# Performance work log

Hardware: AMD Instinct MI355X
Metric: run time of the kernel (lower is better)

The kernel has to match this reference:

```python
import jax, jax.numpy as jnp
import numpy as np

N, T0, T1, C = 65536, 128, 64, 16
MIN_NEAR = 0.05


def _searchsorted(a, v):
    # batched right-side searchsorted over last dim
    return jax.vmap(lambda aa, vv: jnp.searchsorted(aa, vv, side='right'))(a, v)


def contract(x):
    # MERF-style contraction, x: [..., 3]
    ax = jnp.abs(x)
    mag = jnp.max(ax, axis=-1, keepdims=True)              # [..., 1]
    idx = jnp.argmax(ax, axis=-1)                          # [...]
    oh = jnp.arange(x.shape[-1]) == idx[..., None]         # one-hot of max axis
    inv = 1.0 / mag
    scale = jnp.where(oh, (2.0 - inv) * inv, inv)
    return jnp.where(mag < 1.0, x, x * scale)


def sample_pdf(bins, weights, T):
    # bins: [N, T0+1], weights: [N, T0] -> new bins [N, T]
    n, t0 = weights.shape
    w = weights + 0.01
    pdf = w / jnp.sum(w, -1, keepdims=True)
    cdf = jnp.minimum(jnp.cumsum(pdf, -1), 1.0)
    cdf = jnp.concatenate([jnp.zeros_like(cdf[..., :1]), cdf], -1)  # [N, T0+1]
    u = jnp.linspace(0.5 / T, 1.0 - 0.5 / T, T, dtype=bins.dtype)
    u = jnp.broadcast_to(u, (n, T))
    inds = _searchsorted(cdf, u)
    below = jnp.clip(inds - 1, 0, t0)
    above = jnp.clip(inds, 0, t0)
    g = lambda a, i: jnp.take_along_axis(a, i, axis=-1)
    cdf0, cdf1 = g(cdf, below), g(cdf, above)
    b0, b1 = g(bins, below), g(bins, above)
    t = jnp.clip(jnp.nan_to_num((u - cdf0) / (cdf1 - cdf0)), 0.0, 1.0)
    return b0 + t * (b1 - b0)


def compute_weights(real_bins, sigmas):
    deltas = real_bins[..., 1:] - real_bins[..., :-1]
    ds = deltas * sigmas
    alphas = 1.0 - jnp.exp(-ds)
    trans = jnp.exp(-jnp.concatenate(
        [jnp.zeros_like(ds[..., :1]), jnp.cumsum(ds[..., :-1], -1)], -1))
    return jnp.nan_to_num(alphas * trans)


def loss_interlevel(t0, w0, t1, w1):
    cw1 = jnp.concatenate([jnp.zeros_like(w1[..., :1]), jnp.cumsum(w1, -1)], -1)
    hi_clip = w1.shape[-1] - 1
    inds_lo = jnp.clip(_searchsorted(t1[..., :-1], t0[..., :-1]) - 1, 0, hi_clip)
    inds_hi = jnp.clip(_searchsorted(t1[..., 1:], t0[..., 1:]), 0, hi_clip)
    cw1_lo = jnp.take_along_axis(cw1[..., :-1], inds_lo, axis=-1)
    cw1_hi = jnp.take_along_axis(cw1[..., 1:], inds_hi, axis=-1)
    w = cw1_hi - cw1_lo
    return jnp.maximum(w0 - w, 0.0) ** 2 / (w0 + 1e-8)


def eff_distloss(w, m, interval):
    # efficient O(T) distortion loss (torch_efficient_distloss)
    loss_uni = (1.0 / 3.0) * jnp.mean(jnp.sum(interval * w ** 2, -1))
    wm = w * m
    w_cs = jnp.cumsum(w, -1)
    wm_cs = jnp.cumsum(wm, -1)
    loss_bi = 2.0 * jnp.mean(jnp.sum(
        wm[..., 1:] * w_cs[..., :-1] - w[..., 1:] * wm_cs[..., :-1], -1))
    return loss_uni + loss_bi


def setup_inputs():
    key = jax.random.key(0)
    ks = jax.random.split(key, 8)
    rays_o = 0.1 * jax.random.normal(ks[0], (N, 3), jnp.float32)
    rd = jax.random.normal(ks[1], (N, 3), jnp.float32)
    rays_d = rd / jnp.linalg.norm(rd, axis=-1, keepdims=True)
    aabb = jnp.array([-2.0, -2.0, -2.0, 2.0, 2.0, 2.0], jnp.float32)
    sigmas_coarse = 5.0 * jax.random.uniform(ks[2], (N, T0), jnp.float32)
    sigmas_fine = 5.0 * jax.random.uniform(ks[3], (N, T1), jnp.float32)
    colors = jax.random.uniform(ks[4], (N, T1, C), jnp.float32)
    w_view = 0.1 * jax.random.normal(ks[5], (C, 3), jnp.float32)
    b_view = jnp.zeros((3,), jnp.float32)
    return dict(rays_o=rays_o, rays_d=rays_d, aabb=aabb,
                sigmas_coarse=sigmas_coarse, sigmas_fine=sigmas_fine,
                colors=colors, w_view=w_view, b_view=b_view)


def reference(rays_o, rays_d, aabb, sigmas_coarse, sigmas_fine, colors, w_view, b_view):
    # near/far from aabb
    tmin = (aabb[:3] - rays_o) / (rays_d + 1e-15)
    tmax = (aabb[3:] - rays_o) / (rays_d + 1e-15)
    near = jnp.max(jnp.minimum(tmin, tmax), -1, keepdims=True)
    far = jnp.min(jnp.maximum(tmin, tmax), -1, keepdims=True)
    bad = far < near
    near = jnp.maximum(jnp.where(bad, 1e9, near), MIN_NEAR)
    far = jnp.where(bad, 1e9, far)

    spacing = lambda x: jnp.where(x < 1.0, x / 2.0, 1.0 - 1.0 / (2.0 * x))
    spacing_inv = lambda x: jnp.where(x < 0.5, 2.0 * x, 1.0 / (2.0 - 2.0 * x))
    s_near, s_far = spacing(near), spacing(far)

    # coarse (proposal) level: uniform bins in warped space
    bins0 = jnp.broadcast_to(jnp.linspace(0.0, 1.0, T0 + 1, dtype=rays_o.dtype), (N, T0 + 1))
    real_bins0 = spacing_inv(s_near * (1.0 - bins0) + s_far * bins0)
    weights0 = compute_weights(real_bins0, sigmas_coarse)

    # fine level: inverse-CDF sampling (detached in original)
    bins1 = sample_pdf(jax.lax.stop_gradient(bins0),
                       jax.lax.stop_gradient(weights0), T1 + 1)
    real_bins1 = spacing_inv(s_near * (1.0 - bins1) + s_far * bins1)
    rays_t = 0.5 * (real_bins1[..., 1:] + real_bins1[..., :-1])      # [N, T1]
    xyzs = rays_o[:, None, :] + rays_d[:, None, :] * rays_t[..., None]
    xyzs = contract(xyzs)                                            # [N, T1, 3]
    weights1 = compute_weights(real_bins1, sigmas_fine)

    weights_sum = jnp.sum(weights1, -1)                              # [N]
    depth = jnp.sum(weights1 * rays_t, -1)                           # [N]
    f_image = jnp.sum(weights1[..., None] * colors, -2)              # [N, C]
    image = jax.nn.sigmoid(f_image @ w_view + b_view)                # [N, 3]
    image = image + (1.0 - weights_sum)[:, None] * 1.0               # bg_color = 1
    f_xyz = jnp.sum(weights1[..., None] * xyzs, -2)                  # [N, 3]

    prop_loss = jnp.mean(loss_interlevel(
        jax.lax.stop_gradient(bins1), jax.lax.stop_gradient(weights1),
        bins0, weights0))
    intervals = bins1[..., 1:] - bins1[..., :-1]
    mids = bins1[..., :-1] + intervals / 2.0
    dist_loss = eff_distloss(weights1, mids, intervals)

    return image, depth, f_xyz, prop_loss, dist_loss
```

## Files before the change

kernel.cpp:

```cpp
#include <hip/hip_runtime.h>
#include <math.h>

#define NRAYS 65536
#define T0N 128
#define T1N 64
#define CN 16
#define RPB 4
#define NBLK (NRAYS / RPB)

#define IMG_OFF   0
#define DEPTH_OFF (NRAYS * 3)
#define FXYZ_OFF  (NRAYS * 4)
#define PROP_OFF  (NRAYS * 7)
#define DIST_OFF  (NRAYS * 7 + 1)

__device__ __forceinline__ float wave_sum(float x) {
#pragma unroll
  for (int off = 1; off < 64; off <<= 1) x += __shfl_xor(x, off, 64);
  return x;
}

__device__ __forceinline__ float scan_incl(float x, int lane) {
#pragma unroll
  for (int off = 1; off < 64; off <<= 1) {
    float y = __shfl_up(x, off, 64);
    if (lane >= off) x += y;
  }
  return x;
}

__device__ __forceinline__ float spacing_fn(float x) {
  return (x < 1.0f) ? (x * 0.5f) : (1.0f - 1.0f / (2.0f * x));
}
__device__ __forceinline__ float spacing_inv_fn(float x) {
  return (x < 0.5f) ? (2.0f * x) : (1.0f / (2.0f - 2.0f * x));
}

__device__ __forceinline__ int ss_right(const float* a, int n, float v) {
  int lo = 0, hi = n;
  while (lo < hi) {
    int m = (lo + hi) >> 1;
    if (a[m] <= v) lo = m + 1; else hi = m;
  }
  return lo;
}

__global__ void __launch_bounds__(256) nerf_main(
    const float* __restrict__ rays_o, const float* __restrict__ rays_d,
    const float* __restrict__ aabb, const float* __restrict__ sig_c,
    const float* __restrict__ sig_f, const float* __restrict__ colors,
    const float* __restrict__ w_view, const float* __restrict__ b_view,
    float* __restrict__ out, float* __restrict__ ws_partials, int use_atomic) {
  __shared__ float s_cdf[RPB][129 + 1];
  __shared__ float s_bins1[RPB][66];
  __shared__ float s_rb1[RPB][66];
  __shared__ float s_w1[RPB][64];
  __shared__ float s_cw1[RPB][66];
  __shared__ float s_fimg[RPB][16];
  __shared__ float s_scal[RPB][2];

  const int wv = threadIdx.x >> 6;
  const int lane = threadIdx.x & 63;
  const int ray = blockIdx.x * RPB + wv;

  float ro[3], rd[3];
#pragma unroll
  for (int c = 0; c < 3; ++c) { ro[c] = rays_o[ray * 3 + c]; rd[c] = rays_d[ray * 3 + c]; }
  float near = -3.0e38f, far = 3.0e38f;
#pragma unroll
  for (int c = 0; c < 3; ++c) {
    float dd = rd[c] + 1e-15f;
    float ta = (aabb[c] - ro[c]) / dd;
    float tb = (aabb[c + 3] - ro[c]) / dd;
    near = fmaxf(near, fminf(ta, tb));
    far = fminf(far, fmaxf(ta, tb));
  }
  if (far < near) { near = 1e9f; far = 1e9f; }
  near = fmaxf(near, 0.05f);
  const float s_near = spacing_fn(near), s_far = spacing_fn(far);

  const int i0 = 2 * lane, i1 = 2 * lane + 1;
  const float b_a = (float)i0 * (1.0f / 128.0f);
  const float b_b = (float)i1 * (1.0f / 128.0f);
  const float b_c = (float)(i1 + 1) * (1.0f / 128.0f);
  const float rb_a = spacing_inv_fn(s_near * (1.0f - b_a) + s_far * b_a);
  const float rb_b = spacing_inv_fn(s_near * (1.0f - b_b) + s_far * b_b);
  const float rb_c = spacing_inv_fn(s_near * (1.0f - b_c) + s_far * b_c);
  const float2 sg = ((const float2*)sig_c)[ray * 64 + lane];
  const float ds0 = (rb_b - rb_a) * sg.x;
  const float ds1 = (rb_c - rb_b) * sg.y;
  {
  }
  float pr = ds0 + ds1;
  float Spr = scan_incl(pr, lane);
  float E0 = Spr - pr;
  float w00 = (1.0f - expf(-ds0)) * expf(-E0);
  float w01 = (1.0f - expf(-ds1)) * expf(-(E0 + ds0));
  if (w00 != w00) w00 = 0.0f;
  if (w01 != w01) w01 = 0.0f;

  const float wp0 = w00 + 0.01f, wp1 = w01 + 0.01f;
  const float tot = wave_sum(wp0 + wp1);
  const float pdf0 = wp0 / tot, pdf1 = wp1 / tot;
  float prp = pdf0 + pdf1;
  float Sp = scan_incl(prp, lane);
  float Ep = Sp - prp;
  s_cdf[wv][i0 + 1] = fminf(Ep + pdf0, 1.0f);
  s_cdf[wv][i1 + 1] = fminf(Sp, 1.0f);
  if (lane == 0) s_cdf[wv][0] = 0.0f;
  __syncthreads();

  auto sample_one = [&](int j) {
    const float u = ((float)j + 0.5f) * (1.0f / 65.0f);
    int inds = ss_right(&s_cdf[wv][0], 129, u);
    int below = max(min(inds - 1, 128), 0);
    int above = min(inds, 128);
    float c0 = s_cdf[wv][below], c1 = s_cdf[wv][above];
    float b0 = (float)below * (1.0f / 128.0f);
    float b1 = (float)above * (1.0f / 128.0f);
    float t = (u - c0) / (c1 - c0);
    t = fminf(fmaxf(t, 0.0f), 1.0f);
    float bvv = b0 + t * (b1 - b0);
    s_bins1[wv][j] = bvv;
    s_rb1[wv][j] = spacing_inv_fn(s_near * (1.0f - bvv) + s_far * bvv);
  };
  sample_one(lane);
  if (lane == 63) sample_one(64);
  __syncthreads();

  const float rbl = s_rb1[wv][lane];
  const float rbl1 = s_rb1[wv][lane + 1];
  const float delta = rbl1 - rbl;
  const float sgf = sig_f[ray * 64 + lane];
  const float dsf = delta * sgf;
  const float Sf = scan_incl(dsf, lane);
  float w1 = (1.0f - expf(-dsf)) * expf(-(Sf - dsf));
  if (w1 != w1) w1 = 0.0f;
  const float tmid = 0.5f * (rbl + rbl1);

  float px = ro[0] + rd[0] * tmid;
  float py = ro[1] + rd[1] * tmid;
  float pz = ro[2] + rd[2] * tmid;
  float cx = px, cy = py, cz = pz;
  {
    float ax = fabsf(px), ay = fabsf(py), az = fabsf(pz);
    float mag = fmaxf(ax, fmaxf(ay, az));
    if (mag >= 1.0f) {
      float inv = 1.0f / mag;
      float so = (2.0f - inv) * inv;
      int idx = (ax >= ay && ax >= az) ? 0 : ((ay >= az) ? 1 : 2);
      cx = px * (idx == 0 ? so : inv);
      cy = py * (idx == 1 ? so : inv);
      cz = pz * (idx == 2 ? so : inv);
    }
  }

  const float wsum = wave_sum(w1);
  const float depth = wave_sum(w1 * tmid);
  const float fx = wave_sum(w1 * cx);
  const float fy = wave_sum(w1 * cy);
  const float fz = wave_sum(w1 * cz);

  s_w1[wv][lane] = w1;
  const float Scw = scan_incl(w1, lane);
  s_cw1[wv][lane + 1] = Scw;
  if (lane == 0) s_cw1[wv][0] = 0.0f;

  const float bl = s_bins1[wv][lane];
  const float bl1 = s_bins1[wv][lane + 1];
  const float interval = bl1 - bl;
  const float mid = bl + interval * 0.5f;
  const float wm = w1 * mid;
  const float Swm = scan_incl(wm, lane);
  const float w_excl = Scw - w1;
  const float wm_excl = Swm - wm;
  const float dl = (1.0f / 3.0f) * (interval * w1 * w1) + 2.0f * (wm * w_excl - w1 * wm_excl);
  const float dist_part = wave_sum(dl);
  __syncthreads();

  float prop_lane = 0.0f;
  {
    const float* b1p = &s_bins1[wv][0];
    const float* cwp = &s_cw1[wv][0];
#pragma unroll
    for (int k = 0; k < 2; ++k) {
      int i = 2 * lane + k;
      float w0v = (k == 0) ? w00 : w01;
      float vlo = (float)i * (1.0f / 128.0f);
      float vhi = (float)(i + 1) * (1.0f / 128.0f);
      int ilo = max(min(ss_right(b1p, 64, vlo) - 1, 63), 0);
      int ihi = min(ss_right(b1p + 1, 64, vhi), 63);
      float wint = cwp[ihi + 1] - cwp[ilo];
      float diff = fmaxf(w0v - wint, 0.0f);
      prop_lane += diff * diff / (w0v + 1e-8f);
    }
  }
  const float prop_part = wave_sum(prop_lane);

  {
    const int tg = lane >> 2, cg = lane & 3;
    const float4* col4 = (const float4*)(colors + (size_t)ray * (T1N * CN));
    float a0 = 0.f, a1 = 0.f, a2 = 0.f, a3 = 0.f;
#pragma unroll
    for (int it = 0; it < 4; ++it) {
      int t = tg + 16 * it;
      float wvv = s_w1[wv][t];
      float4 cvv = col4[t * 4 + cg];
      a0 = fmaf(wvv, cvv.x, a0);
      a1 = fmaf(wvv, cvv.y, a1);
      a2 = fmaf(wvv, cvv.z, a2);
      a3 = fmaf(wvv, cvv.w, a3);
    }
#pragma unroll
    for (int m = 4; m < 64; m <<= 1) {
      a0 += __shfl_xor(a0, m, 64);
      a1 += __shfl_xor(a1, m, 64);
      a2 += __shfl_xor(a2, m, 64);
      a3 += __shfl_xor(a3, m, 64);
    }
    if (lane < 4) {
      s_fimg[wv][lane * 4 + 0] = a0;
      s_fimg[wv][lane * 4 + 1] = a1;
      s_fimg[wv][lane * 4 + 2] = a2;
      s_fimg[wv][lane * 4 + 3] = a3;
    }
  }
  __syncthreads();

  if (lane < 3) {
    float acc = b_view[lane];
#pragma unroll
    for (int c = 0; c < 16; ++c) acc = fmaf(s_fimg[wv][c], w_view[c * 3 + lane], acc);
    out[IMG_OFF + ray * 3 + lane] = 1.0f / (1.0f + expf(-acc)) + (1.0f - wsum);
    out[FXYZ_OFF + ray * 3 + lane] = (lane == 0) ? fx : ((lane == 1) ? fy : fz);
  }
  if (lane == 0) {
    out[DEPTH_OFF + ray] = depth;
    s_scal[wv][0] = prop_part;
    s_scal[wv][1] = dist_part;
  }
  __syncthreads();
  if (threadIdx.x == 0) {
    float P = s_scal[0][0] + s_scal[1][0] + s_scal[2][0] + s_scal[3][0];
    float D = s_scal[0][1] + s_scal[1][1] + s_scal[2][1] + s_scal[3][1];
    if (use_atomic) {
      atomicAdd(out + PROP_OFF, P * (1.0f / ((float)NRAYS * 128.0f)));
      atomicAdd(out + DIST_OFF, D * (1.0f / (float)NRAYS));
    } else {
      ws_partials[blockIdx.x] = P;
      ws_partials[NBLK + blockIdx.x] = D;
    }
  }
}

__global__ void __launch_bounds__(256) reduce_partials(const float* __restrict__ ws,
                                                       float* __restrict__ out) {
  float p = 0.0f, d = 0.0f;
  for (int i = threadIdx.x; i < NBLK; i += 256) {
    p += ws[i];
    d += ws[NBLK + i];
  }
  p = wave_sum(p);
  d = wave_sum(d);
  __shared__ float sp[4], sd[4];
  const int wv = threadIdx.x >> 6, lane = threadIdx.x & 63;
  if (lane == 0) { sp[wv] = p; sd[wv] = d; }
  __syncthreads();
  if (threadIdx.x == 0) {
    float P = sp[0] + sp[1] + sp[2] + sp[3];
    float D = sd[0] + sd[1] + sd[2] + sd[3];
    out[PROP_OFF] = P * (1.0f / ((float)NRAYS * 128.0f));
    out[DIST_OFF] = D * (1.0f / (float)NRAYS);
  }
}

extern "C" void kernel_launch(void* const* d_in, const int* in_sizes, int n_in,
                              void* d_out, int out_size, void* d_ws, size_t ws_size,
                              hipStream_t stream) {
  const float* rays_o = (const float*)d_in[0];
  const float* rays_d = (const float*)d_in[1];
  const float* aabb = (const float*)d_in[2];
  const float* sig_c = (const float*)d_in[3];
  const float* sig_f = (const float*)d_in[4];
  const float* colors = (const float*)d_in[5];
  const float* w_view = (const float*)d_in[6];
  const float* b_view = (const float*)d_in[7];
  float* out = (float*)d_out;
  float* wsf = (float*)d_ws;

  const bool use_ws = (ws_size >= (size_t)(2 * NBLK) * sizeof(float)) && (wsf != nullptr);
  if (!use_ws) {
    hipMemsetAsync(out + PROP_OFF, 0, 2 * sizeof(float), stream);
  }
  nerf_main<<<NBLK, 256, 0, stream>>>(rays_o, rays_d, aabb, sig_c, sig_f, colors,
                                      w_view, b_view, out, wsf, use_ws ? 0 : 1);
  if (use_ws) reduce_partials<<<1, 256, 0, stream>>>(wsf, out);
}
```

Baseline: 439.5 us.

## Replace block barriers with wave-level syncs, shuffles, and early global loads

Each wavefront handles one ray, so the block-wide __syncthreads become wave barriers with an LDS fence. Several shared arrays are replaced by register shuffles: bins, real bins, w1 for the color sum, and f_image for the view projection. The colors and sigma loads are hoisted to the kernel start so their latency overlaps the coarse-pass math, and the normalization now reuses a single scan plus a reciprocal. Fast __expf replaces expf, which changes rounding slightly, and the partials reduction is vectorized.

```diff
diff --git a/kernel.cpp b/kernel.cpp
--- a/kernel.cpp
+++ b/kernel.cpp
@@ -29,6 +29,12 @@
   return x;
 }
 
+__device__ __forceinline__ void wave_lds_sync() {
+  __builtin_amdgcn_wave_barrier();
+  __builtin_amdgcn_fence(__ATOMIC_ACQ_REL, "workgroup");
+  __builtin_amdgcn_wave_barrier();
+}
+
 __device__ __forceinline__ float spacing_fn(float x) {
   return (x < 1.0f) ? (x * 0.5f) : (1.0f - 1.0f / (2.0f * x));
 }
@@ -51,17 +57,23 @@
     const float* __restrict__ sig_f, const float* __restrict__ colors,
     const float* __restrict__ w_view, const float* __restrict__ b_view,
     float* __restrict__ out, float* __restrict__ ws_partials, int use_atomic) {
-  __shared__ float s_cdf[RPB][129 + 1];
-  __shared__ float s_bins1[RPB][66];
-  __shared__ float s_rb1[RPB][66];
-  __shared__ float s_w1[RPB][64];
-  __shared__ float s_cw1[RPB][66];
-  __shared__ float s_fimg[RPB][16];
+  __shared__ float s_cdf[RPB][130];
+  __shared__ float s_bins1[RPB][65];
+  __shared__ float s_cw1[RPB][65];
   __shared__ float s_scal[RPB][2];
 
   const int wv = threadIdx.x >> 6;
   const int lane = threadIdx.x & 63;
   const int ray = blockIdx.x * RPB + wv;
+
+  const int tg = lane >> 2, cg = lane & 3;
+  const float4* col4 = (const float4*)(colors + (size_t)ray * (T1N * CN));
+  const float4 cva = col4[(tg + 0) * 4 + cg];
+  const float4 cvb = col4[(tg + 16) * 4 + cg];
+  const float4 cvc = col4[(tg + 32) * 4 + cg];
+  const float4 cvd = col4[(tg + 48) * 4 + cg];
+  const float2 sg = ((const float2*)sig_c)[ray * 64 + lane];
+  const float sgf = sig_f[ray * 64 + lane];
 
   float ro[3], rd[3];
 #pragma unroll
@@ -86,31 +98,28 @@
   const float rb_a = spacing_inv_fn(s_near * (1.0f - b_a) + s_far * b_a);
   const float rb_b = spacing_inv_fn(s_near * (1.0f - b_b) + s_far * b_b);
   const float rb_c = spacing_inv_fn(s_near * (1.0f - b_c) + s_far * b_c);
-  const float2 sg = ((const float2*)sig_c)[ray * 64 + lane];
   const float ds0 = (rb_b - rb_a) * sg.x;
   const float ds1 = (rb_c - rb_b) * sg.y;
-  {
-  }
-  float pr = ds0 + ds1;
-  float Spr = scan_incl(pr, lane);
-  float E0 = Spr - pr;
-  float w00 = (1.0f - expf(-ds0)) * expf(-E0);
-  float w01 = (1.0f - expf(-ds1)) * expf(-(E0 + ds0));
+  const float pr = ds0 + ds1;
+  const float Spr = scan_incl(pr, lane);
+  const float E0 = Spr - pr;
+  const float e0 = __expf(-E0);
+  const float ed0 = __expf(-ds0);
+  float w00 = (1.0f - ed0) * e0;
+  float w01 = (1.0f - __expf(-ds1)) * (e0 * ed0);
   if (w00 != w00) w00 = 0.0f;
   if (w01 != w01) w01 = 0.0f;
 
   const float wp0 = w00 + 0.01f, wp1 = w01 + 0.01f;
-  const float tot = wave_sum(wp0 + wp1);
-  const float pdf0 = wp0 / tot, pdf1 = wp1 / tot;
-  float prp = pdf0 + pdf1;
-  float Sp = scan_incl(prp, lane);
-  float Ep = Sp - prp;
-  s_cdf[wv][i0 + 1] = fminf(Ep + pdf0, 1.0f);
-  s_cdf[wv][i1 + 1] = fminf(Sp, 1.0f);
+  const float S2 = scan_incl(wp0 + wp1, lane);
+  const float tot = __shfl(S2, 63, 64);
+  const float rt = 1.0f / tot;
+  s_cdf[wv][i0 + 1] = fminf((S2 - wp1) * rt, 1.0f);
+  s_cdf[wv][i1 + 1] = fminf(S2 * rt, 1.0f);
   if (lane == 0) s_cdf[wv][0] = 0.0f;
-  __syncthreads();
-
-  auto sample_one = [&](int j) {
+  wave_lds_sync();
+
+  auto sample_one = [&](int j) -> float {
     const float u = ((float)j + 0.5f) * (1.0f / 65.0f);
     int inds = ss_right(&s_cdf[wv][0], 129, u);
     int below = max(min(inds - 1, 128), 0);
@@ -122,19 +131,19 @@
     t = fminf(fmaxf(t, 0.0f), 1.0f);
     float bvv = b0 + t * (b1 - b0);
     s_bins1[wv][j] = bvv;
-    s_rb1[wv][j] = spacing_inv_fn(s_near * (1.0f - bvv) + s_far * bvv);
+    return bvv;
   };
-  sample_one(lane);
-  if (lane == 63) sample_one(64);
-  __syncthreads();
-
-  const float rbl = s_rb1[wv][lane];
-  const float rbl1 = s_rb1[wv][lane + 1];
-  const float delta = rbl1 - rbl;
-  const float sgf = sig_f[ray * 64 + lane];
-  const float dsf = delta * sgf;
+  const float bv = sample_one(lane);
+  float bv64 = 0.0f;
+  if (lane == 63) bv64 = sample_one(64);
+  float bvn = __shfl_down(bv, 1, 64);
+  if (lane == 63) bvn = bv64;
+
+  const float rbl  = spacing_inv_fn(s_near * (1.0f - bv)  + s_far * bv);
+  const float rbl1 = spacing_inv_fn(s_near * (1.0f - bvn) + s_far * bvn);
+  const float dsf = (rbl1 - rbl) * sgf;
   const float Sf = scan_incl(dsf, lane);
-  float w1 = (1.0f - expf(-dsf)) * expf(-(Sf - dsf));
+  float w1 = (1.0f - __expf(-dsf)) * __expf(-(Sf - dsf));
   if (w1 != w1) w1 = 0.0f;
   const float tmid = 0.5f * (rbl + rbl1);
 
@@ -155,28 +164,23 @@
     }
   }
 
-  const float wsum = wave_sum(w1);
+  const float Scw = scan_incl(w1, lane);
+  const float wsum = __shfl(Scw, 63, 64);
   const float depth = wave_sum(w1 * tmid);
   const float fx = wave_sum(w1 * cx);
   const float fy = wave_sum(w1 * cy);
   const float fz = wave_sum(w1 * cz);
-
-  s_w1[wv][lane] = w1;
-  const float Scw = scan_incl(w1, lane);
   s_cw1[wv][lane + 1] = Scw;
   if (lane == 0) s_cw1[wv][0] = 0.0f;
 
-  const float bl = s_bins1[wv][lane];
-  const float bl1 = s_bins1[wv][lane + 1];
-  const float interval = bl1 - bl;
-  const float mid = bl + interval * 0.5f;
+  const float interval = bvn - bv;
+  const float mid = bv + interval * 0.5f;
   const float wm = w1 * mid;
   const float Swm = scan_incl(wm, lane);
-  const float w_excl = Scw - w1;
-  const float wm_excl = Swm - wm;
-  const float dl = (1.0f / 3.0f) * (interval * w1 * w1) + 2.0f * (wm * w_excl - w1 * wm_excl);
+  const float dl = (1.0f / 3.0f) * (interval * w1 * w1) +
+                   2.0f * (wm * (Scw - w1) - w1 * (Swm - wm));
   const float dist_part = wave_sum(dl);
-  __syncthreads();
+  wave_lds_sync();
 
   float prop_lane = 0.0f;
   {
@@ -197,20 +201,16 @@
   }
   const float prop_part = wave_sum(prop_lane);
 
+  float a0, a1, a2, a3;
   {
-    const int tg = lane >> 2, cg = lane & 3;
-    const float4* col4 = (const float4*)(colors + (size_t)ray * (T1N * CN));
-    float a0 = 0.f, a1 = 0.f, a2 = 0.f, a3 = 0.f;
-#pragma unroll
-    for (int it = 0; it < 4; ++it) {
-      int t = tg + 16 * it;
-      float wvv = s_w1[wv][t];
-      float4 cvv = col4[t * 4 + cg];
-      a0 = fmaf(wvv, cvv.x, a0);
-      a1 = fmaf(wvv, cvv.y, a1);
-      a2 = fmaf(wvv, cvv.z, a2);
-      a3 = fmaf(wvv, cvv.w, a3);
-    }
+    const float wv0 = __shfl(w1, tg, 64);
+    const float wv1 = __shfl(w1, tg + 16, 64);
+    const float wv2 = __shfl(w1, tg + 32, 64);
+    const float wv3 = __shfl(w1, tg + 48, 64);
+    a0 = fmaf(wv0, cva.x, fmaf(wv1, cvb.x, fmaf(wv2, cvc.x, wv3 * cvd.x)));
+    a1 = fmaf(wv0, cva.y, fmaf(wv1, cvb.y, fmaf(wv2, cvc.y, wv3 * cvd.y)));
+    a2 = fmaf(wv0, cva.z, fmaf(wv1, cvb.z, fmaf(wv2, cvc.z, wv3 * cvd.z)));
+    a3 = fmaf(wv0, cva.w, fmaf(wv1, cvb.w, fmaf(wv2, cvc.w, wv3 * cvd.w)));
 #pragma unroll
     for (int m = 4; m < 64; m <<= 1) {
       a0 += __shfl_xor(a0, m, 64);
@@ -218,20 +218,26 @@
       a2 += __shfl_xor(a2, m, 64);
       a3 += __shfl_xor(a3, m, 64);
     }
-    if (lane < 4) {
-      s_fimg[wv][lane * 4 + 0] = a0;
-      s_fimg[wv][lane * 4 + 1] = a1;
-      s_fimg[wv][lane * 4 + 2] = a2;
-      s_fimg[wv][lane * 4 + 3] = a3;
-    }
-  }
-  __syncthreads();
+  }
+  float acc0 = 0.f, acc1 = 0.f, acc2 = 0.f;
+  {
+    const int ch = cg * 4;
+    const float* wvp = w_view + ch * 3;
+    acc0 = fmaf(a0, wvp[0], fmaf(a1, wvp[3], fmaf(a2, wvp[6], a3 * wvp[9])));
+    acc1 = fmaf(a0, wvp[1], fmaf(a1, wvp[4], fmaf(a2, wvp[7], a3 * wvp[10])));
+    acc2 = fmaf(a0, wvp[2], fmaf(a1, wvp[5], fmaf(a2, wvp[8], a3 * wvp[11])));
+#pragma unroll
+    for (int m = 1; m < 4; m <<= 1) {
+      acc0 += __shfl_xor(acc0, m, 64);
+      acc1 += __shfl_xor(acc1, m, 64);
+      acc2 += __shfl_xor(acc2, m, 64);
+    }
+  }
 
   if (lane < 3) {
-    float acc = b_view[lane];
-#pragma unroll
-    for (int c = 0; c < 16; ++c) acc = fmaf(s_fimg[wv][c], w_view[c * 3 + lane], acc);
-    out[IMG_OFF + ray * 3 + lane] = 1.0f / (1.0f + expf(-acc)) + (1.0f - wsum);
+    float acc = (lane == 0) ? acc0 : ((lane == 1) ? acc1 : acc2);
+    acc += b_view[lane];
+    out[IMG_OFF + ray * 3 + lane] = 1.0f / (1.0f + __expf(-acc)) + (1.0f - wsum);
     out[FXYZ_OFF + ray * 3 + lane] = (lane == 0) ? fx : ((lane == 1) ? fy : fz);
   }
   if (lane == 0) {
@@ -255,10 +261,13 @@
 
 __global__ void __launch_bounds__(256) reduce_partials(const float* __restrict__ ws,
                                                        float* __restrict__ out) {
+  const float4* w4 = (const float4*)ws;
   float p = 0.0f, d = 0.0f;
-  for (int i = threadIdx.x; i < NBLK; i += 256) {
-    p += ws[i];
-    d += ws[NBLK + i];
+  for (int i = threadIdx.x; i < NBLK / 4; i += 256) {
+    float4 a = w4[i];
+    p += (a.x + a.y) + (a.z + a.w);
+    float4 b = w4[NBLK / 4 + i];
+    d += (b.x + b.y) + (b.z + b.w);
   }
   p = wave_sum(p);
   d = wave_sum(d);
```

Measured after the change: 410.7 us. -6.6%, faster.
